# Performance work log

Measured on AMD Instinct MI355X. Metric: run time of the kernel, lower is better.

Reference implementation:

```python
import jax, jax.numpy as jnp
import numpy as np

B, D, H, W, K = 32, 64, 64, 64, 512  # batch, embed_dim (channels), latent HxW, codebook size
BETA = 0.2


def setup_inputs() -> dict:
    key = jax.random.key(0)
    k1, k2 = jax.random.split(key)
    features = jax.random.normal(k1, (B, D, H, W), dtype=jnp.float32)
    emb_weight = jax.random.normal(k2, (K, D), dtype=jnp.float32)
    return {"features": features, "emb_weight": emb_weight}


def reference(features, emb_weight):
    b, d, h, w = features.shape
    # NCHW -> (B, HW, D) channels-last flatten (torch permute(0,2,3,1).view)
    quant_in = features.transpose(0, 2, 3, 1).reshape(b, h * w, d)
    # squared euclidean distances (argmin-equivalent to torch.cdist)
    x2 = jnp.sum(quant_in * quant_in, axis=-1, keepdims=True)          # (B, HW, 1)
    e2 = jnp.sum(emb_weight * emb_weight, axis=-1)                     # (K,)
    dist2 = x2 + e2[None, None, :] - 2.0 * jnp.einsum('bnd,kd->bnk', quant_in, emb_weight)
    min_index = jnp.argmin(dist2, axis=-1)                             # (B, HW)
    quant_out = emb_weight[min_index]                                  # gather, (B, HW, D)
    # commitment + beta * codebook loss (means over all elements)
    commitment_loss = jnp.mean((jax.lax.stop_gradient(quant_out) - quant_in) ** 2)
    codebook_loss = jnp.mean((quant_out - jax.lax.stop_gradient(quant_in)) ** 2)
    quantize_loss = commitment_loss + BETA * codebook_loss
    # straight-through estimator
    st = quant_in + jax.lax.stop_gradient(quant_out - quant_in)
    st = st.reshape(b, h, w, d).transpose(0, 3, 1, 2)                  # back to NCHW
    return st, quantize_loss
```

## Files before the change

kernel.cpp:

```cpp
#include <hip/hip_runtime.h>
#include <hip/hip_bf16.h>

#define BB 32
#define DD 64
#define HWHW 4096
#define NPOS 131072
#define NELEM (NPOS * DD)
#define KK 512
#define LOSS_SCALE (1.2f / 8388608.f)
#define DELTA 1.5f
#define QCAP 6144

typedef __attribute__((ext_vector_type(8))) short short8v;
typedef __attribute__((ext_vector_type(4))) float float4v;

__device__ inline unsigned short f2bf(float f) {
    unsigned u = __float_as_uint(f);
    unsigned r = u + 0x7FFFu + ((u >> 16) & 1u);
    return (unsigned short)(r >> 16);
}
__device__ inline float bf2f(unsigned short s) {
    return __uint_as_float(((unsigned)s) << 16);
}
__device__ inline unsigned f2o(float f) {
    unsigned u = __float_as_uint(f);
    return ((int)u < 0) ? ~u : (u | 0x80000000u);
}

__global__ __launch_bounds__(256) void vq_prep(const float* __restrict__ emb,
                                               unsigned short* __restrict__ ebf,
                                               float* __restrict__ e2h) {
    const int t = blockIdx.x * 256 + threadIdx.x;
    const int row = t >> 4, c = t & 15;
    const float4 v = *(const float4*)(emb + row * DD + c * 4);
    unsigned u0 = (unsigned)f2bf(v.x) | ((unsigned)f2bf(v.y) << 16);
    unsigned u1 = (unsigned)f2bf(v.z) | ((unsigned)f2bf(v.w) << 16);
    *(uint2*)(ebf + row * DD + c * 4) = make_uint2(u0, u1);
    float p = v.x * v.x + v.y * v.y + v.z * v.z + v.w * v.w;
    p += __shfl_xor(p, 1, 64); p += __shfl_xor(p, 2, 64);
    p += __shfl_xor(p, 4, 64); p += __shfl_xor(p, 8, 64);
    if (c == 0) e2h[row] = 0.5f * p;
}

__global__ __launch_bounds__(256, 1) void vq_main(
        const float* __restrict__ feat,
        const float* __restrict__ emb,
        const unsigned short* __restrict__ ebf,
        const float* __restrict__ e2h,
        float* __restrict__ out,
        float* __restrict__ loss) {

    __shared__ unsigned long long sbest[512];
    __shared__ unsigned qbuf[QCAP];
    __shared__ unsigned qcnt;
    __shared__ float wsum[4];

    const int tid = threadIdx.x;
    const int wid = tid >> 6, lane = tid & 63;
    const int l15 = lane & 15, lg = lane >> 4;

    sbest[tid] = 0ull; sbest[tid + 256] = 0ull;
    if (tid == 0) qcnt = 0u;

    const int pbase = blockIdx.x * 512;
    const int b     = pbase >> 12;
    const int hwb   = pbase & 4095;
    const float* featB = feat + (size_t)b * DD * HWHW;
    float*       outB  = out  + (size_t)b * DD * HWHW;
    const int wbase = wid * 128;

    short8v bx[8][2];
#pragma unroll
    for (int pt = 0; pt < 8; ++pt) {
        const int hw = hwb + wbase + pt * 16 + l15;
#pragma unroll
        for (int h = 0; h < 2; ++h) {
            float xv[8];
#pragma unroll
            for (int j = 0; j < 8; ++j) {
                const int d = h * 32 + lg * 8 + j;
                xv[j] = featB[(size_t)d * HWHW + hw];
            }
            short8v s;
#pragma unroll
            for (int j = 0; j < 8; ++j) s[j] = (short)f2bf(xv[j]);
            bx[pt][h] = s;
        }
    }

    __syncthreads();

    const char* ebfB = (const char*)ebf;

    float M[8];
#pragma unroll
    for (int pt = 0; pt < 8; ++pt) M[pt] = -3.0e38f;

    short8v a0n = *(const short8v*)(ebfB + l15 * 128 + lg * 16);
    short8v a1n = *(const short8v*)(ebfB + l15 * 128 + 64 + lg * 16);
    float4v e2n = *(const float4v*)(e2h + lg * 4);

    for (int ct = 0; ct < 32; ++ct) {
        const short8v a0c = a0n, a1c = a1n;
        float4v nege2;
#pragma unroll
        for (int r = 0; r < 4; ++r) nege2[r] = -e2n[r];
        if (ct < 31) {
            const char* p = ebfB + ((ct + 1) * 16 + l15) * 128 + lg * 16;
            a0n = *(const short8v*)p;
            a1n = *(const short8v*)(p + 64);
            e2n = *(const float4v*)(e2h + (ct + 1) * 16 + lg * 4);
        }
        float4v acc[8];
#pragma unroll
        for (int pt = 0; pt < 8; ++pt)
            acc[pt] = __builtin_amdgcn_mfma_f32_16x16x32_bf16(a0c, bx[pt][0], nege2, 0, 0, 0);
#pragma unroll
        for (int pt = 0; pt < 8; ++pt)
            acc[pt] = __builtin_amdgcn_mfma_f32_16x16x32_bf16(a1c, bx[pt][1], acc[pt], 0, 0, 0);
#pragma unroll
        for (int pt = 0; pt < 8; ++pt) {
            const float m01 = fmaxf(acc[pt][0], acc[pt][1]);
            const float m23 = fmaxf(acc[pt][2], acc[pt][3]);
            M[pt] = fmaxf(M[pt], fmaxf(m01, m23));
        }
    }

    float thr[8];
#pragma unroll
    for (int pt = 0; pt < 8; ++pt) {
        float m = M[pt];
        m = fmaxf(m, __shfl_xor(m, 16, 64));
        m = fmaxf(m, __shfl_xor(m, 32, 64));
        thr[pt] = m - DELTA;
    }

    a0n = *(const short8v*)(ebfB + l15 * 128 + lg * 16);
    a1n = *(const short8v*)(ebfB + l15 * 128 + 64 + lg * 16);
    e2n = *(const float4v*)(e2h + lg * 4);

    for (int ct = 0; ct < 32; ++ct) {
        const short8v a0c = a0n, a1c = a1n;
        float4v nege2;
#pragma unroll
        for (int r = 0; r < 4; ++r) nege2[r] = -e2n[r];
        if (ct < 31) {
            const char* p = ebfB + ((ct + 1) * 16 + l15) * 128 + lg * 16;
            a0n = *(const short8v*)p;
            a1n = *(const short8v*)(p + 64);
            e2n = *(const float4v*)(e2h + (ct + 1) * 16 + lg * 4);
        }
        float4v acc[8];
#pragma unroll
        for (int pt = 0; pt < 8; ++pt)
            acc[pt] = __builtin_amdgcn_mfma_f32_16x16x32_bf16(a0c, bx[pt][0], nege2, 0, 0, 0);
#pragma unroll
        for (int pt = 0; pt < 8; ++pt)
            acc[pt] = __builtin_amdgcn_mfma_f32_16x16x32_bf16(a1c, bx[pt][1], acc[pt], 0, 0, 0);
#pragma unroll
        for (int pt = 0; pt < 8; ++pt) {
            const float m01 = fmaxf(acc[pt][0], acc[pt][1]);
            const float m23 = fmaxf(acc[pt][2], acc[pt][3]);
            const float mx  = fmaxf(m01, m23);
            if (__any(mx >= thr[pt])) {
#pragma unroll
                for (int r = 0; r < 4; ++r) {
                    if (acc[pt][r] >= thr[pt]) {
                        const unsigned idx  = atomicAdd(&qcnt, 1u);
                        const unsigned code = (unsigned)(ct * 16 + lg * 4 + r);
                        const unsigned pos  = (unsigned)(wbase + pt * 16 + l15);
                        if (idx < QCAP) qbuf[idx] = (pos << 9) | code;
                    }
                }
            }
        }
    }

    __syncthreads();

    const unsigned nq = min(qcnt, (unsigned)QCAP);
    for (unsigned i = tid; i < nq; i += 256) {
        const unsigned e = qbuf[i];
        const unsigned p = e >> 9, k = e & 511u;
        const float* er = emb + k * DD;
        float a0 = 0.f, a1 = 0.f, a2 = 0.f, a3 = 0.f;
#pragma unroll
        for (int d = 0; d < DD; d += 4) {
            a0 = fmaf(featB[(size_t)(d    ) * HWHW + hwb + p], er[d    ], a0);
            a1 = fmaf(featB[(size_t)(d + 1) * HWHW + hwb + p], er[d + 1], a1);
            a2 = fmaf(featB[(size_t)(d + 2) * HWHW + hwb + p], er[d + 2], a2);
            a3 = fmaf(featB[(size_t)(d + 3) * HWHW + hwb + p], er[d + 3], a3);
        }
        const float sc = ((a0 + a1) + (a2 + a3)) - e2h[k];
        const unsigned long long key =
            ((unsigned long long)f2o(sc) << 32) | (unsigned long long)(511u - k);
        atomicMax(&sbest[p], key);
    }

    __syncthreads();

    float lsum = 0.f;
#pragma unroll
    for (int pt = 0; pt < 8; ++pt) {
        const int pl = wbase + pt * 16 + l15;
        const int hw = hwb + pl;
        const unsigned long long key = sbest[pl];
        const unsigned k = 511u - (unsigned)key;
        const float* er = emb + k * DD;
#pragma unroll
        for (int h = 0; h < 2; ++h) {
            const short8v xs = bx[pt][h];
#pragma unroll
            for (int jj = 0; jj < 2; ++jj) {
                const float4v ev = *(const float4v*)(er + h * 32 + lg * 8 + jj * 4);
#pragma unroll
                for (int c = 0; c < 4; ++c) {
                    const int j = jj * 4 + c;
                    const int d = h * 32 + lg * 8 + j;
                    const float q = ev[c];
                    outB[(size_t)d * HWHW + hw] = q;
                    const float diff = q - bf2f((unsigned short)xs[j]);
                    lsum = fmaf(diff, diff, lsum);
                }
            }
        }
    }

#pragma unroll
    for (int off = 32; off > 0; off >>= 1) lsum += __shfl_down(lsum, off, 64);
    if (lane == 0) wsum[wid] = lsum;
    __syncthreads();
    if (tid == 0)
        atomicAdd(loss, (wsum[0] + wsum[1] + wsum[2] + wsum[3]) * LOSS_SCALE);
}

extern "C" void kernel_launch(void* const* d_in, const int* in_sizes, int n_in,
                              void* d_out, int out_size, void* d_ws, size_t ws_size,
                              hipStream_t stream) {
    const float* feat = (const float*)d_in[0];
    const float* emb  = (const float*)d_in[1];
    float* out  = (float*)d_out;
    float* loss = out + NELEM;

    unsigned short* ebf = (unsigned short*)d_ws;
    float*          e2h = (float*)((char*)d_ws + 64 * 1024);

    hipMemsetAsync(loss, 0, sizeof(float), stream);
    vq_prep<<<dim3(32), dim3(256), 0, stream>>>(emb, ebf, e2h);
    vq_main<<<dim3(256), dim3(256), 0, stream>>>(feat, emb, ebf, e2h, out, loss);
}
```

Measured before the change: 165.8 us.

## Shrink per-block position tile to raise grid size and occupancy

Each block now handles 128 positions instead of 512, so the grid grows from 256 to 1024 blocks and launch bounds allow 4 blocks per CU. The aim is to fill all CUs of the GPU and hide memory latency with more resident waves. The negated half-norm is precomputed in the prep kernel, which removes a per-tile negation. The candidate margin is widened and the queue capacity reduced. The codebook is reloaded by four times as many blocks, and each wave now has fewer MFMA tiles per codebook fetch, which lowers reuse. Queue overflow is also more likely, since the wider margin queues more candidates into a smaller buffer.

Measured after the change: 191.4 us. +15.4%, slower.

```diff
diff --git a/kernel.cpp b/kernel.cpp
--- a/kernel.cpp
+++ b/kernel.cpp
@@ -8,8 +8,11 @@
 #define NELEM (NPOS * DD)
 #define KK 512
 #define LOSS_SCALE (1.2f / 8388608.f)
-#define DELTA 1.5f
-#define QCAP 6144
+#define DELTA 2.0f
+#define QCAP 2048
+#define PT 2
+#define POSB 128
+#define NBLK (NPOS / POSB)
 
 typedef __attribute__((ext_vector_type(8))) short short8v;
 typedef __attribute__((ext_vector_type(4))) float float4v;
@@ -29,7 +32,7 @@
 
 __global__ __launch_bounds__(256) void vq_prep(const float* __restrict__ emb,
                                                unsigned short* __restrict__ ebf,
-                                               float* __restrict__ e2h) {
+                                               float* __restrict__ ne2h) {
     const int t = blockIdx.x * 256 + threadIdx.x;
     const int row = t >> 4, c = t & 15;
     const float4 v = *(const float4*)(emb + row * DD + c * 4);
@@ -39,18 +42,18 @@
     float p = v.x * v.x + v.y * v.y + v.z * v.z + v.w * v.w;
     p += __shfl_xor(p, 1, 64); p += __shfl_xor(p, 2, 64);
     p += __shfl_xor(p, 4, 64); p += __shfl_xor(p, 8, 64);
-    if (c == 0) e2h[row] = 0.5f * p;
-}
-
-__global__ __launch_bounds__(256, 1) void vq_main(
+    if (c == 0) ne2h[row] = -0.5f * p;
+}
+
+__global__ __launch_bounds__(256, 4) void vq_main(
         const float* __restrict__ feat,
         const float* __restrict__ emb,
         const unsigned short* __restrict__ ebf,
-        const float* __restrict__ e2h,
+        const float* __restrict__ ne2h,
         float* __restrict__ out,
         float* __restrict__ loss) {
 
-    __shared__ unsigned long long sbest[512];
+    __shared__ unsigned long long sbest[POSB];
     __shared__ unsigned qbuf[QCAP];
     __shared__ unsigned qcnt;
     __shared__ float wsum[4];
@@ -59,19 +62,19 @@
     const int wid = tid >> 6, lane = tid & 63;
     const int l15 = lane & 15, lg = lane >> 4;
 
-    sbest[tid] = 0ull; sbest[tid + 256] = 0ull;
+    if (tid < POSB) sbest[tid] = 0ull;
     if (tid == 0) qcnt = 0u;
 
-    const int pbase = blockIdx.x * 512;
+    const int pbase = blockIdx.x * POSB;
     const int b     = pbase >> 12;
     const int hwb   = pbase & 4095;
     const float* featB = feat + (size_t)b * DD * HWHW;
     float*       outB  = out  + (size_t)b * DD * HWHW;
-    const int wbase = wid * 128;
-
-    short8v bx[8][2];
-#pragma unroll
-    for (int pt = 0; pt < 8; ++pt) {
+    const int wbase = wid * (PT * 16);
+
+    short8v bx[PT][2];
+#pragma unroll
+    for (int pt = 0; pt < PT; ++pt) {
         const int hw = hwb + wbase + pt * 16 + l15;
 #pragma unroll
         for (int h = 0; h < 2; ++h) {
@@ -92,43 +95,41 @@
 
     const char* ebfB = (const char*)ebf;
 
-    float M[8];
-#pragma unroll
-    for (int pt = 0; pt < 8; ++pt) M[pt] = -3.0e38f;
+    float M[PT];
+#pragma unroll
+    for (int pt = 0; pt < PT; ++pt) M[pt] = -3.0e38f;
 
     short8v a0n = *(const short8v*)(ebfB + l15 * 128 + lg * 16);
     short8v a1n = *(const short8v*)(ebfB + l15 * 128 + 64 + lg * 16);
-    float4v e2n = *(const float4v*)(e2h + lg * 4);
+    float4v ne2n = *(const float4v*)(ne2h + lg * 4);
 
     for (int ct = 0; ct < 32; ++ct) {
         const short8v a0c = a0n, a1c = a1n;
-        float4v nege2;
-#pragma unroll
-        for (int r = 0; r < 4; ++r) nege2[r] = -e2n[r];
+        const float4v ne2c = ne2n;
         if (ct < 31) {
             const char* p = ebfB + ((ct + 1) * 16 + l15) * 128 + lg * 16;
             a0n = *(const short8v*)p;
             a1n = *(const short8v*)(p + 64);
-            e2n = *(const float4v*)(e2h + (ct + 1) * 16 + lg * 4);
-        }
-        float4v acc[8];
-#pragma unroll
-        for (int pt = 0; pt < 8; ++pt)
-            acc[pt] = __builtin_amdgcn_mfma_f32_16x16x32_bf16(a0c, bx[pt][0], nege2, 0, 0, 0);
-#pragma unroll
-        for (int pt = 0; pt < 8; ++pt)
+            ne2n = *(const float4v*)(ne2h + (ct + 1) * 16 + lg * 4);
+        }
+        float4v acc[PT];
+#pragma unroll
+        for (int pt = 0; pt < PT; ++pt)
+            acc[pt] = __builtin_amdgcn_mfma_f32_16x16x32_bf16(a0c, bx[pt][0], ne2c, 0, 0, 0);
+#pragma unroll
+        for (int pt = 0; pt < PT; ++pt)
             acc[pt] = __builtin_amdgcn_mfma_f32_16x16x32_bf16(a1c, bx[pt][1], acc[pt], 0, 0, 0);
 #pragma unroll
-        for (int pt = 0; pt < 8; ++pt) {
+        for (int pt = 0; pt < PT; ++pt) {
             const float m01 = fmaxf(acc[pt][0], acc[pt][1]);
             const float m23 = fmaxf(acc[pt][2], acc[pt][3]);
             M[pt] = fmaxf(M[pt], fmaxf(m01, m23));
         }
     }
 
-    float thr[8];
-#pragma unroll
-    for (int pt = 0; pt < 8; ++pt) {
+    float thr[PT];
+#pragma unroll
+    for (int pt = 0; pt < PT; ++pt) {
         float m = M[pt];
         m = fmaxf(m, __shfl_xor(m, 16, 64));
         m = fmaxf(m, __shfl_xor(m, 32, 64));
@@ -137,28 +138,26 @@
 
     a0n = *(const short8v*)(ebfB + l15 * 128 + lg * 16);
     a1n = *(const short8v*)(ebfB + l15 * 128 + 64 + lg * 16);
-    e2n = *(const float4v*)(e2h + lg * 4);
+    ne2n = *(const float4v*)(ne2h + lg * 4);
 
     for (int ct = 0; ct < 32; ++ct) {
         const short8v a0c = a0n, a1c = a1n;
-        float4v nege2;
-#pragma unroll
-        for (int r = 0; r < 4; ++r) nege2[r] = -e2n[r];
+        const float4v ne2c = ne2n;
         if (ct < 31) {
             const char* p = ebfB + ((ct + 1) * 16 + l15) * 128 + lg * 16;
             a0n = *(const short8v*)p;
             a1n = *(const short8v*)(p + 64);
-            e2n = *(const float4v*)(e2h + (ct + 1) * 16 + lg * 4);
-        }
-        float4v acc[8];
-#pragma unroll
-        for (int pt = 0; pt < 8; ++pt)
-            acc[pt] = __builtin_amdgcn_mfma_f32_16x16x32_bf16(a0c, bx[pt][0], nege2, 0, 0, 0);
-#pragma unroll
-        for (int pt = 0; pt < 8; ++pt)
+            ne2n = *(const float4v*)(ne2h + (ct + 1) * 16 + lg * 4);
+        }
+        float4v acc[PT];
+#pragma unroll
+        for (int pt = 0; pt < PT; ++pt)
+            acc[pt] = __builtin_amdgcn_mfma_f32_16x16x32_bf16(a0c, bx[pt][0], ne2c, 0, 0, 0);
+#pragma unroll
+        for (int pt = 0; pt < PT; ++pt)
             acc[pt] = __builtin_amdgcn_mfma_f32_16x16x32_bf16(a1c, bx[pt][1], acc[pt], 0, 0, 0);
 #pragma unroll
-        for (int pt = 0; pt < 8; ++pt) {
+        for (int pt = 0; pt < PT; ++pt) {
             const float m01 = fmaxf(acc[pt][0], acc[pt][1]);
             const float m23 = fmaxf(acc[pt][2], acc[pt][3]);
             const float mx  = fmaxf(m01, m23);
@@ -191,7 +190,7 @@
             a2 = fmaf(featB[(size_t)(d + 2) * HWHW + hwb + p], er[d + 2], a2);
             a3 = fmaf(featB[(size_t)(d + 3) * HWHW + hwb + p], er[d + 3], a3);
         }
-        const float sc = ((a0 + a1) + (a2 + a3)) - e2h[k];
+        const float sc = ((a0 + a1) + (a2 + a3)) + ne2h[k];
         const unsigned long long key =
             ((unsigned long long)f2o(sc) << 32) | (unsigned long long)(511u - k);
         atomicMax(&sbest[p], key);
@@ -201,7 +200,7 @@
 
     float lsum = 0.f;
 #pragma unroll
-    for (int pt = 0; pt < 8; ++pt) {
+    for (int pt = 0; pt < PT; ++pt) {
         const int pl = wbase + pt * 16 + l15;
         const int hw = hwb + pl;
         const unsigned long long key = sbest[pl];
@@ -242,10 +241,10 @@
     float* out  = (float*)d_out;
     float* loss = out + NELEM;
 
-    unsigned short* ebf = (unsigned short*)d_ws;
-    float*          e2h = (float*)((char*)d_ws + 64 * 1024);
+    unsigned short* ebf  = (unsigned short*)d_ws;
+    float*          ne2h = (float*)((char*)d_ws + 64 * 1024);
 
     hipMemsetAsync(loss, 0, sizeof(float), stream);
-    vq_prep<<<dim3(32), dim3(256), 0, stream>>>(emb, ebf, e2h);
-    vq_main<<<dim3(256), dim3(256), 0, stream>>>(feat, emb, ebf, e2h, out, loss);
-}
+    vq_prep<<<dim3(32), dim3(256), 0, stream>>>(emb, ebf, ne2h);
+    vq_main<<<dim3(NBLK), dim3(256), 0, stream>>>(feat, emb, ebf, ne2h, out, loss);
+}
```
